# Optimization experiments

Measured on AMD Instinct MI355X. Metric: run time of the kernel, lower is better.

The kernel has to match this reference:

```python
import jax, jax.numpy as jnp
import numpy as np

DT = 0.001  # euler step size (module default dt)
T = 2000    # num_timesteps
N_IN = 8192
N_OUT = 4096


def setup_inputs() -> dict:
    key = jax.random.key(0)
    k_x, k_w = jax.random.split(key)
    x = jax.random.normal(k_x, (T, N_IN), dtype=jnp.float32)
    # module initializes weight.data.uniform_(-0.1, 0.1)
    weight = jax.random.uniform(k_w, (N_OUT, N_IN), dtype=jnp.float32, minval=-0.1, maxval=0.1)
    ones = jnp.ones((N_OUT,), dtype=jnp.float32)
    # default_lif_parameters broadcast to per-neuron vectors (constant_lif_parameters)
    return {
        "x": x,
        "weight": weight,
        "v_th": ones * 75.0,
        "v_rest": ones * 50.0,
        "v_reset": ones * 30.0,
        "t_ref": ones * 0.001,
        "tau": ones * 2.0,
    }


def reference(x, weight, v_th, v_rest, v_reset, t_ref, tau):
    # lif_input[t] = x[t] @ weight.T  -> [T, N_OUT]
    lif_input = x @ weight.T

    def step(carry, inp):
        v, refrac = carry
        # leak toward v_rest
        v = v - DT * tau * (v - v_rest)
        # integrate input only when not refractory
        v = v + jnp.where(refrac == 0, inp, jnp.zeros_like(inp))
        # count down refractory period
        refrac = jnp.where(refrac > 0, refrac - DT, jnp.zeros_like(refrac))
        # heavyside spike
        spike = (v - v_th >= 0).astype(v.dtype)
        sb = spike > 0
        # reset: refractory period and membrane potential
        refrac = jnp.where(sb, t_ref, refrac)
        v = jnp.where(sb, v_reset, v)
        return (v, refrac), spike

    v0 = v_rest.astype(x.dtype)               # v[0] = v_rest
    refrac0 = jnp.zeros_like(v0)
    # torch loop runs i = 1 .. T-1 consuming lif_input[i]
    _, spikes = jax.lax.scan(step, (v0, refrac0), lif_input[1:])
    s0 = jnp.zeros((1, spikes.shape[1]), dtype=spikes.dtype)  # s[0] stays zero
    return jnp.concatenate([s0, spikes], axis=0)  # [T, N_OUT]
```

## Files before the change

### kernel.cpp

```cpp
#include <hip/hip_runtime.h>
#include <hip/hip_bf16.h>


#define T_STEPS 2000
#define NIN_K   8192
#define NOUT_N  4096
#define MPAD    2048

typedef __attribute__((ext_vector_type(8))) _Float16 half8;
typedef __attribute__((ext_vector_type(4))) float f32x4;

#define GLL16(g, l)                                                              \
    __builtin_amdgcn_global_load_lds(                                            \
        (const __attribute__((address_space(1))) void*)(g),                      \
        (__attribute__((address_space(3))) void*)(l), 16, 0, 0)

__global__ __launch_bounds__(256) void split_f32(const float* __restrict__ src,
                                                 _Float16* __restrict__ hi,
                                                 _Float16* __restrict__ lo,
                                                 size_t n_valid) {
    const size_t i8 = (size_t)(blockIdx.x * 256u + threadIdx.x) * 8;
    float vv[8];
    if (i8 < n_valid) {
        float4 v0 = *(const float4*)(src + i8);
        float4 v1 = *(const float4*)(src + i8 + 4);
        vv[0] = v0.x; vv[1] = v0.y; vv[2] = v0.z; vv[3] = v0.w;
        vv[4] = v1.x; vv[5] = v1.y; vv[6] = v1.z; vv[7] = v1.w;
    } else {
#pragma unroll
        for (int j = 0; j < 8; ++j) vv[j] = 0.f;
    }
    half8 h8, l8;
#pragma unroll
    for (int j = 0; j < 8; ++j) {
        _Float16 h = (_Float16)vv[j];
        float r = __fsub_rn(vv[j], (float)h);
        h8[j] = h;
        l8[j] = (_Float16)(r * 4096.0f);
    }
    *(half8*)(hi + i8) = h8;
    *(half8*)(lo + i8) = l8;
}

__global__ __launch_bounds__(512, 2) void gemm_f16x2(const _Float16* __restrict__ A0,
                                                     const _Float16* __restrict__ A1,
                                                     const _Float16* __restrict__ B0,
                                                     const _Float16* __restrict__ B1,
                                                     float* __restrict__ C) {
    __shared__ _Float16 lds[2][4][128 * 64];

    const int tid  = threadIdx.x;
    const int wave = tid >> 6;
    const int lane = tid & 63;
    const int bm = blockIdx.y * 128;
    const int bn = blockIdx.x * 128;
    const int wm = (wave >> 2) * 64;
    const int wn = (wave & 3) * 32;

    const int sr0 = wave * 16 + (lane >> 3);
    const int sr1 = sr0 + 8;
    const int sc0 = ((lane & 7) ^ (sr0 & 7)) * 8;
    const int sc1 = ((lane & 7) ^ (sr1 & 7)) * 8;
    const _Float16* pa00 = A0 + (size_t)(bm + sr0) * NIN_K + sc0;
    const _Float16* pa01 = A0 + (size_t)(bm + sr1) * NIN_K + sc1;
    const _Float16* pa10 = A1 + (size_t)(bm + sr0) * NIN_K + sc0;
    const _Float16* pa11 = A1 + (size_t)(bm + sr1) * NIN_K + sc1;
    const _Float16* pb00 = B0 + (size_t)(bn + sr0) * NIN_K + sc0;
    const _Float16* pb01 = B0 + (size_t)(bn + sr1) * NIN_K + sc1;
    const _Float16* pb10 = B1 + (size_t)(bn + sr0) * NIN_K + sc0;
    const _Float16* pb11 = B1 + (size_t)(bn + sr1) * NIN_K + sc1;
    const int ldsOff0 = (wave * 16) * 64;
    const int ldsOff1 = (wave * 16 + 8) * 64;

    f32x4 acc0[4][2], acc1[4][2];
#pragma unroll
    for (int i = 0; i < 4; ++i)
#pragma unroll
        for (int j = 0; j < 2; ++j) {
            acc0[i][j] = (f32x4){0.f, 0.f, 0.f, 0.f};
            acc1[i][j] = (f32x4){0.f, 0.f, 0.f, 0.f};
        }

    const int quad = lane >> 4;
    const int l16  = lane & 15;

#define STAGE(BUF)                                                               \
    {                                                                            \
        GLL16(pa00, &lds[BUF][0][ldsOff0]); GLL16(pa01, &lds[BUF][0][ldsOff1]);  \
        GLL16(pa10, &lds[BUF][1][ldsOff0]); GLL16(pa11, &lds[BUF][1][ldsOff1]);  \
        GLL16(pb00, &lds[BUF][2][ldsOff0]); GLL16(pb01, &lds[BUF][2][ldsOff1]);  \
        GLL16(pb10, &lds[BUF][3][ldsOff0]); GLL16(pb11, &lds[BUF][3][ldsOff1]);  \
        pa00 += 64; pa01 += 64; pa10 += 64; pa11 += 64;                          \
        pb00 += 64; pb01 += 64; pb10 += 64; pb11 += 64;                          \
    }

#define WAIT8  asm volatile("s_waitcnt vmcnt(8)" ::: "memory")
#define WAIT0  asm volatile("s_waitcnt vmcnt(0)" ::: "memory")
#define BARRIER                                                                  \
    {                                                                            \
        __builtin_amdgcn_s_barrier();                                            \
        __builtin_amdgcn_sched_barrier(0);                                       \
    }

#define COMPUTE(BUF)                                                             \
    _Pragma("unroll") for (int ks = 0; ks < 2; ++ks) {                           \
        half8 b0f[2], b1f[2];                                                    \
        _Pragma("unroll") for (int j = 0; j < 2; ++j) {                          \
            const int row = wn + j * 16 + l16;                                   \
            const int off = row * 64 + ((ks * 4 + quad) ^ (row & 7)) * 8;        \
            b0f[j] = *(const half8*)&lds[BUF][2][off];                           \
            b1f[j] = *(const half8*)&lds[BUF][3][off];                           \
        }                                                                        \
        _Pragma("unroll") for (int i = 0; i < 4; ++i) {                          \
            const int row = wm + i * 16 + l16;                                   \
            const int off = row * 64 + ((ks * 4 + quad) ^ (row & 7)) * 8;        \
            const half8 a0f = *(const half8*)&lds[BUF][0][off];                  \
            const half8 a1f = *(const half8*)&lds[BUF][1][off];                  \
            _Pragma("unroll") for (int j = 0; j < 2; ++j) {                      \
                acc0[i][j] = __builtin_amdgcn_mfma_f32_16x16x32_f16(a0f, b0f[j], acc0[i][j], 0, 0, 0); \
                acc1[i][j] = __builtin_amdgcn_mfma_f32_16x16x32_f16(a0f, b1f[j], acc1[i][j], 0, 0, 0); \
                acc1[i][j] = __builtin_amdgcn_mfma_f32_16x16x32_f16(a1f, b0f[j], acc1[i][j], 0, 0, 0); \
            }                                                                    \
        }                                                                        \
    }

    STAGE(0)

#pragma unroll 1
    for (int t = 0; t < 126; t += 2) {
        STAGE(1)
        WAIT8;
        BARRIER
        COMPUTE(0)
        BARRIER
        STAGE(0)
        WAIT8;
        BARRIER
        COMPUTE(1)
        BARRIER
    }
    STAGE(1)
    WAIT8;
    BARRIER
    COMPUTE(0)
    WAIT0;
    BARRIER
    COMPUTE(1)

#undef STAGE
#undef WAIT8
#undef WAIT0
#undef BARRIER
#undef COMPUTE

    const float s = 1.0f / 4096.0f;
#pragma unroll
    for (int i = 0; i < 4; ++i)
#pragma unroll
        for (int j = 0; j < 2; ++j) {
            const int m = bm + wm + i * 16 + quad * 4;
            const int n = bn + wn + j * 16 + l16;
            float* cp = C + (size_t)m * NOUT_N + n;
#pragma unroll
            for (int r = 0; r < 4; ++r)
                cp[(size_t)r * NOUT_N] = __fmaf_rn(acc1[i][j][r], s, acc0[i][j][r]);
        }
}

#define BM 64
#define BN 64
#define BK 16
#define PAD 4
__global__ __launch_bounds__(256) void gemm_bt(const float* __restrict__ A,
                                               const float* __restrict__ B,
                                               float* __restrict__ C,
                                               int M, int N, int K) {
    __shared__ float As[BK][BM + PAD];
    __shared__ float Bs[BK][BN + PAD];
    const int bm = blockIdx.y * BM, bn = blockIdx.x * BN;
    const int tid = threadIdx.x;
    const int tx = tid & 15, ty = tid >> 4;
    const int lrow = tid >> 2, lk = (tid & 3) * 4;
    float acc[4][4];
#pragma unroll
    for (int i = 0; i < 4; ++i)
#pragma unroll
        for (int j = 0; j < 4; ++j) acc[i][j] = 0.0f;
    for (int k0 = 0; k0 < K; k0 += BK) {
        const int am = bm + lrow;
        float4 av = (am < M) ? *(const float4*)(A + (size_t)am * K + k0 + lk)
                             : make_float4(0.f, 0.f, 0.f, 0.f);
        As[lk + 0][lrow] = av.x; As[lk + 1][lrow] = av.y;
        As[lk + 2][lrow] = av.z; As[lk + 3][lrow] = av.w;
        float4 bv = *(const float4*)(B + (size_t)(bn + lrow) * K + k0 + lk);
        Bs[lk + 0][lrow] = bv.x; Bs[lk + 1][lrow] = bv.y;
        Bs[lk + 2][lrow] = bv.z; Bs[lk + 3][lrow] = bv.w;
        __syncthreads();
#pragma unroll
        for (int k = 0; k < BK; ++k) {
            float a[4], b[4];
#pragma unroll
            for (int i = 0; i < 4; ++i) a[i] = As[k][ty * 4 + i];
#pragma unroll
            for (int j = 0; j < 4; ++j) b[j] = Bs[k][tx * 4 + j];
#pragma unroll
            for (int i = 0; i < 4; ++i)
#pragma unroll
                for (int j = 0; j < 4; ++j) acc[i][j] += a[i] * b[j];
        }
        __syncthreads();
    }
#pragma unroll
    for (int i = 0; i < 4; ++i) {
        const int m = bm + ty * 4 + i;
        if (m < M) {
            float* cp = C + (size_t)m * N + bn + tx * 4;
#pragma unroll
            for (int j = 0; j < 4; ++j) cp[j] = acc[i][j];
        }
    }
}

__global__ void zero_rows(float* __restrict__ p, size_t n) {
    const size_t i = (size_t)blockIdx.x * 256 + threadIdx.x;
    if (i < n) p[i] = 0.0f;
}

__global__ __launch_bounds__(64) void lif_scan(const float* __restrict__ inp,
                                               const float* __restrict__ v_th_p,
                                               const float* __restrict__ v_rest_p,
                                               const float* __restrict__ v_reset_p,
                                               const float* __restrict__ t_ref_p,
                                               const float* __restrict__ tau_p,
                                               float* __restrict__ out) {
    const int lane = threadIdx.x;
    const int j = blockIdx.x * 64 + lane;

    const float vth = v_th_p[j], vrest = v_rest_p[j], vres = v_reset_p[j];
    const float tref = t_ref_p[j];
    const float cleak = __fmul_rn(0.001f, tau_p[j]);
    float v = vrest, refrac = 0.0f;
    out[j] = 0.0f;

    const float* plv = inp + (size_t)1 * NOUT_N + j;
    float* pst = out + (size_t)1 * NOUT_N + j;

    float p00, p01, p02, p03, p04, p05, p06, p07, p08, p09, p10, p11, p12, p13, p14, p15;
    float p16, p17, p18, p19, p20, p21, p22, p23, p24, p25, p26, p27, p28, p29, p30, p31;

#define LDP(PD)                                                                   \
    asm volatile("global_load_dword %0, %1, off" : "=v"(PD) : "v"(plv) : "memory"); \
    plv += NOUT_N;

#define STEPA(PD, WSTR)                                                           \
    {                                                                             \
        asm volatile(WSTR : "+v"(PD)::"memory");                                  \
        const float in = PD;                                                      \
        const float dd = __fmul_rn(cleak, __fsub_rn(v, vrest));                   \
        v = __fsub_rn(v, dd);                                                     \
        v = (refrac == 0.0f) ? __fadd_rn(v, in) : v;                              \
        refrac = (refrac > 0.0f) ? (refrac - 0.001f) : 0.0f;                      \
        const bool s = (__fsub_rn(v, vth) >= 0.0f);                               \
        const float spk = s ? 1.0f : 0.0f;                                        \
        asm volatile("global_store_dword %0, %1, off" ::"v"(pst), "v"(spk)        \
                     : "memory");                                                 \
        pst += NOUT_N;                                                            \
        asm volatile("global_load_dword %0, %1, off" : "=v"(PD) : "v"(plv)        \
                     : "memory");                                                 \
        plv += NOUT_N;                                                            \
        refrac = s ? tref : refrac;                                               \
        v = s ? vres : v;                                                         \
    }

#define GROUP32(WSTR)                                                             \
    STEPA(p00, WSTR) STEPA(p01, WSTR) STEPA(p02, WSTR) STEPA(p03, WSTR)           \
    STEPA(p04, WSTR) STEPA(p05, WSTR) STEPA(p06, WSTR) STEPA(p07, WSTR)           \
    STEPA(p08, WSTR) STEPA(p09, WSTR) STEPA(p10, WSTR) STEPA(p11, WSTR)           \
    STEPA(p12, WSTR) STEPA(p13, WSTR) STEPA(p14, WSTR) STEPA(p15, WSTR)           \
    STEPA(p16, WSTR) STEPA(p17, WSTR) STEPA(p18, WSTR) STEPA(p19, WSTR)           \
    STEPA(p20, WSTR) STEPA(p21, WSTR) STEPA(p22, WSTR) STEPA(p23, WSTR)           \
    STEPA(p24, WSTR) STEPA(p25, WSTR) STEPA(p26, WSTR) STEPA(p27, WSTR)           \
    STEPA(p28, WSTR) STEPA(p29, WSTR) STEPA(p30, WSTR) STEPA(p31, WSTR)

#define TAILSTEP(PD)                                                              \
    {                                                                             \
        const float in = PD;                                                      \
        const float dd = __fmul_rn(cleak, __fsub_rn(v, vrest));                   \
        v = __fsub_rn(v, dd);                                                     \
        v = (refrac == 0.0f) ? __fadd_rn(v, in) : v;                              \
        refrac = (refrac > 0.0f) ? (refrac - 0.001f) : 0.0f;                      \
        const bool s = (__fsub_rn(v, vth) >= 0.0f);                               \
        *pst = s ? 1.0f : 0.0f;                                                   \
        pst += NOUT_N;                                                            \
        refrac = s ? tref : refrac;                                               \
        v = s ? vres : v;                                                         \
    }

    LDP(p00) LDP(p01) LDP(p02) LDP(p03) LDP(p04) LDP(p05) LDP(p06) LDP(p07)
    LDP(p08) LDP(p09) LDP(p10) LDP(p11) LDP(p12) LDP(p13) LDP(p14) LDP(p15)
    LDP(p16) LDP(p17) LDP(p18) LDP(p19) LDP(p20) LDP(p21) LDP(p22) LDP(p23)
    LDP(p24) LDP(p25) LDP(p26) LDP(p27) LDP(p28) LDP(p29) LDP(p30) LDP(p31)

    GROUP32("s_waitcnt vmcnt(31)")

#pragma unroll 1
    for (int g = 1; g < 62; ++g) {
        GROUP32("s_waitcnt vmcnt(62)")
    }

    asm volatile("s_waitcnt vmcnt(0)" ::: "memory");
    __builtin_amdgcn_sched_barrier(0);

    TAILSTEP(p00) TAILSTEP(p01) TAILSTEP(p02) TAILSTEP(p03) TAILSTEP(p04)
    TAILSTEP(p05) TAILSTEP(p06) TAILSTEP(p07) TAILSTEP(p08) TAILSTEP(p09)
    TAILSTEP(p10) TAILSTEP(p11) TAILSTEP(p12) TAILSTEP(p13) TAILSTEP(p14)

#undef LDP
#undef STEPA
#undef GROUP32
#undef TAILSTEP
}

extern "C" void kernel_launch(void* const* d_in, const int* in_sizes, int n_in,
                              void* d_out, int out_size, void* d_ws, size_t ws_size,
                              hipStream_t stream) {
    const float* x       = (const float*)d_in[0];
    const float* w       = (const float*)d_in[1];
    const float* v_th    = (const float*)d_in[2];
    const float* v_rest  = (const float*)d_in[3];
    const float* v_reset = (const float*)d_in[4];
    const float* t_ref   = (const float*)d_in[5];
    const float* tau     = (const float*)d_in[6];
    float* out = (float*)d_out;

    const size_t LIF_B = (size_t)MPAD * NOUT_N * 4;
    const size_t XS_B  = (size_t)MPAD * NIN_K * 2;
    const size_t WS_B  = (size_t)NOUT_N * NIN_K * 2;
    const size_t NEED  = LIF_B + 2 * XS_B + 2 * WS_B;

    char* ws = (char*)d_ws;
    float* lif = (float*)ws;

    if (ws_size >= NEED) {
        _Float16* x0 = (_Float16*)(ws + LIF_B);
        _Float16* x1 = (_Float16*)(ws + LIF_B + XS_B);
        _Float16* w0 = (_Float16*)(ws + LIF_B + 2 * XS_B);
        _Float16* w1 = (_Float16*)(ws + LIF_B + 2 * XS_B + WS_B);

        const size_t nx = (size_t)MPAD * NIN_K;
        split_f32<<<nx / 8 / 256, 256, 0, stream>>>(x, x0, x1,
                                                    (size_t)T_STEPS * NIN_K);
        const size_t nw = (size_t)NOUT_N * NIN_K;
        split_f32<<<nw / 8 / 256, 256, 0, stream>>>(w, w0, w1, nw);

        dim3 g(NOUT_N / 128, MPAD / 128);
        gemm_f16x2<<<g, 512, 0, stream>>>(x0, x1, w0, w1, lif);
    } else {
        dim3 g(NOUT_N / BN, (T_STEPS + BM - 1) / BM);
        gemm_bt<<<g, 256, 0, stream>>>(x, w, lif, T_STEPS, NOUT_N, NIN_K);
        const size_t padn = (size_t)(MPAD - T_STEPS) * NOUT_N;
        zero_rows<<<(padn + 255) / 256, 256, 0, stream>>>(lif + (size_t)T_STEPS * NOUT_N, padn);
    }

    lif_scan<<<NOUT_N / 64, 64, 0, stream>>>(lif, v_th, v_rest, v_reset, t_ref, tau, out);
}
```

Before: 733.7 us.

## Use 4-wave 64x64 warp tiles with K=32 stages in split-f16 GEMM

Restructures the split-fp16 GEMM from 8 waves with 64x32 warp tiles to 4 waves with 64x64 warp tiles. Each wave now reuses A and B fragments across more MFMAs, which cuts LDS read traffic per MFMA. The K step per stage is halved to 32 with a new paired-row swizzled LDS layout, and per-lane LDS offsets are precomputed. In exchange it uses twice as many loop iterations and barriers, fewer waves per block, and more accumulator registers, which may lower occupancy.

```diff
diff --git a/kernel.cpp b/kernel.cpp
--- a/kernel.cpp
+++ b/kernel.cpp
@@ -42,47 +42,59 @@
     *(half8*)(lo + i8) = l8;
 }
 
-__global__ __launch_bounds__(512, 2) void gemm_f16x2(const _Float16* __restrict__ A0,
+__global__ __launch_bounds__(256, 2) void gemm_f16x2(const _Float16* __restrict__ A0,
                                                      const _Float16* __restrict__ A1,
                                                      const _Float16* __restrict__ B0,
                                                      const _Float16* __restrict__ B1,
                                                      float* __restrict__ C) {
-    __shared__ _Float16 lds[2][4][128 * 64];
+    __shared__ _Float16 lds[2][4][128 * 32];
 
     const int tid  = threadIdx.x;
     const int wave = tid >> 6;
     const int lane = tid & 63;
     const int bm = blockIdx.y * 128;
     const int bn = blockIdx.x * 128;
-    const int wm = (wave >> 2) * 64;
-    const int wn = (wave & 3) * 32;
-
-    const int sr0 = wave * 16 + (lane >> 3);
-    const int sr1 = sr0 + 8;
-    const int sc0 = ((lane & 7) ^ (sr0 & 7)) * 8;
-    const int sc1 = ((lane & 7) ^ (sr1 & 7)) * 8;
-    const _Float16* pa00 = A0 + (size_t)(bm + sr0) * NIN_K + sc0;
-    const _Float16* pa01 = A0 + (size_t)(bm + sr1) * NIN_K + sc1;
-    const _Float16* pa10 = A1 + (size_t)(bm + sr0) * NIN_K + sc0;
-    const _Float16* pa11 = A1 + (size_t)(bm + sr1) * NIN_K + sc1;
-    const _Float16* pb00 = B0 + (size_t)(bn + sr0) * NIN_K + sc0;
-    const _Float16* pb01 = B0 + (size_t)(bn + sr1) * NIN_K + sc1;
-    const _Float16* pb10 = B1 + (size_t)(bn + sr0) * NIN_K + sc0;
-    const _Float16* pb11 = B1 + (size_t)(bn + sr1) * NIN_K + sc1;
-    const int ldsOff0 = (wave * 16) * 64;
-    const int ldsOff1 = (wave * 16 + 8) * 64;
-
-    f32x4 acc0[4][2], acc1[4][2];
+    const int wm = (wave >> 1) * 64;
+    const int wn = (wave & 1) * 64;
+
+    const int rch = 2 * (lane >> 3) + ((lane >> 2) & 1);
+    const int kh  = ((lane & 3) ^ ((lane >> 3) & 3)) * 8;
+    const int sr0 = wave * 32 + rch;
+    const int sr1 = sr0 + 16;
+    const _Float16* pa00 = A0 + (size_t)(bm + sr0) * NIN_K + kh;
+    const _Float16* pa01 = A0 + (size_t)(bm + sr1) * NIN_K + kh;
+    const _Float16* pa10 = A1 + (size_t)(bm + sr0) * NIN_K + kh;
+    const _Float16* pa11 = A1 + (size_t)(bm + sr1) * NIN_K + kh;
+    const _Float16* pb00 = B0 + (size_t)(bn + sr0) * NIN_K + kh;
+    const _Float16* pb01 = B0 + (size_t)(bn + sr1) * NIN_K + kh;
+    const _Float16* pb10 = B1 + (size_t)(bn + sr0) * NIN_K + kh;
+    const _Float16* pb11 = B1 + (size_t)(bn + sr1) * NIN_K + kh;
+    const int ldsOff0 = (wave * 32) * 32;
+    const int ldsOff1 = (wave * 32 + 16) * 32;
+
+    const int quad = lane >> 4;
+    const int l16  = lane & 15;
+
+    int offA[4], offB[4];
+#pragma unroll
+    for (int i = 0; i < 4; ++i) {
+        const int row = wm + i * 16 + l16;
+        offA[i] = (row >> 1) * 64 + (row & 1) * 32 + ((quad ^ ((row >> 1) & 3))) * 8;
+    }
+#pragma unroll
+    for (int j = 0; j < 4; ++j) {
+        const int row = wn + j * 16 + l16;
+        offB[j] = (row >> 1) * 64 + (row & 1) * 32 + ((quad ^ ((row >> 1) & 3))) * 8;
+    }
+
+    f32x4 acc0[4][4], acc1[4][4];
 #pragma unroll
     for (int i = 0; i < 4; ++i)
 #pragma unroll
-        for (int j = 0; j < 2; ++j) {
+        for (int j = 0; j < 4; ++j) {
             acc0[i][j] = (f32x4){0.f, 0.f, 0.f, 0.f};
             acc1[i][j] = (f32x4){0.f, 0.f, 0.f, 0.f};
         }
-
-    const int quad = lane >> 4;
-    const int l16  = lane & 15;
 
 #define STAGE(BUF)                                                               \
     {                                                                            \
@@ -90,8 +102,8 @@
         GLL16(pa10, &lds[BUF][1][ldsOff0]); GLL16(pa11, &lds[BUF][1][ldsOff1]);  \
         GLL16(pb00, &lds[BUF][2][ldsOff0]); GLL16(pb01, &lds[BUF][2][ldsOff1]);  \
         GLL16(pb10, &lds[BUF][3][ldsOff0]); GLL16(pb11, &lds[BUF][3][ldsOff1]);  \
-        pa00 += 64; pa01 += 64; pa10 += 64; pa11 += 64;                          \
-        pb00 += 64; pb01 += 64; pb10 += 64; pb11 += 64;                          \
+        pa00 += 32; pa01 += 32; pa10 += 32; pa11 += 32;                          \
+        pb00 += 32; pb01 += 32; pb10 += 32; pb11 += 32;                          \
     }
 
 #define WAIT8  asm volatile("s_waitcnt vmcnt(8)" ::: "memory")
@@ -103,20 +115,16 @@
     }
 
 #define COMPUTE(BUF)                                                             \
-    _Pragma("unroll") for (int ks = 0; ks < 2; ++ks) {                           \
-        half8 b0f[2], b1f[2];                                                    \
-        _Pragma("unroll") for (int j = 0; j < 2; ++j) {                          \
-            const int row = wn + j * 16 + l16;                                   \
-            const int off = row * 64 + ((ks * 4 + quad) ^ (row & 7)) * 8;        \
-            b0f[j] = *(const half8*)&lds[BUF][2][off];                           \
-            b1f[j] = *(const half8*)&lds[BUF][3][off];                           \
+    {                                                                            \
+        half8 b0f[4], b1f[4];                                                    \
+        _Pragma("unroll") for (int j = 0; j < 4; ++j) {                          \
+            b0f[j] = *(const half8*)&lds[BUF][2][offB[j]];                       \
+            b1f[j] = *(const half8*)&lds[BUF][3][offB[j]];                       \
         }                                                                        \
         _Pragma("unroll") for (int i = 0; i < 4; ++i) {                          \
-            const int row = wm + i * 16 + l16;                                   \
-            const int off = row * 64 + ((ks * 4 + quad) ^ (row & 7)) * 8;        \
-            const half8 a0f = *(const half8*)&lds[BUF][0][off];                  \
-            const half8 a1f = *(const half8*)&lds[BUF][1][off];                  \
-            _Pragma("unroll") for (int j = 0; j < 2; ++j) {                      \
+            const half8 a0f = *(const half8*)&lds[BUF][0][offA[i]];              \
+            const half8 a1f = *(const half8*)&lds[BUF][1][offA[i]];              \
+            _Pragma("unroll") for (int j = 0; j < 4; ++j) {                      \
                 acc0[i][j] = __builtin_amdgcn_mfma_f32_16x16x32_f16(a0f, b0f[j], acc0[i][j], 0, 0, 0); \
                 acc1[i][j] = __builtin_amdgcn_mfma_f32_16x16x32_f16(a0f, b1f[j], acc1[i][j], 0, 0, 0); \
                 acc1[i][j] = __builtin_amdgcn_mfma_f32_16x16x32_f16(a1f, b0f[j], acc1[i][j], 0, 0, 0); \
@@ -127,7 +135,7 @@
     STAGE(0)
 
 #pragma unroll 1
-    for (int t = 0; t < 126; t += 2) {
+    for (int t = 0; t < 254; t += 2) {
         STAGE(1)
         WAIT8;
         BARRIER
@@ -157,7 +165,7 @@
 #pragma unroll
     for (int i = 0; i < 4; ++i)
 #pragma unroll
-        for (int j = 0; j < 2; ++j) {
+        for (int j = 0; j < 4; ++j) {
             const int m = bm + wm + i * 16 + quad * 4;
             const int n = bn + wn + j * 16 + l16;
             float* cp = C + (size_t)m * NOUT_N + n;
@@ -354,7 +362,7 @@
         split_f32<<<nw / 8 / 256, 256, 0, stream>>>(w, w0, w1, nw);
 
         dim3 g(NOUT_N / 128, MPAD / 128);
-        gemm_f16x2<<<g, 512, 0, stream>>>(x0, x1, w0, w1, lif);
+        gemm_f16x2<<<g, 256, 0, stream>>>(x0, x1, w0, w1, lif);
     } else {
         dim3 g(NOUT_N / BN, (T_STEPS + BM - 1) / BM);
         gemm_bt<<<g, 256, 0, stream>>>(x, w, lif, T_STEPS, NOUT_N, NIN_K);
```

Result: slower. 784.3 us (+6.9%).
